# Optimization experiments

Hardware: AMD Instinct MI355X
Metric: run time of the kernel (lower is better)

## Reference

```python
import jax, jax.numpy as jnp
import numpy as np

# Broyden low-rank inverse-Jacobian matvecs. Us: [b,d,e,T], VTs: [b,T,d,e], x: [b,d,e].
# Unwritten history slots are zero, so using the full buffers equals torch's :nstep slicing.

def _matvec(Us, VTs, x):
    VTx = jnp.einsum('btde,bde->bt', VTs, x)
    return -x + jnp.einsum('bdet,bt->bde', Us, VTx)

def _rmatvec(Us, VTs, x):
    xTU = jnp.einsum('bde,bdet->bt', x, Us)
    return -x + jnp.einsum('bt,btde->bde', xTU, VTs)

def broyden(g, x0, threshold, eps):
    """Faithful port of broyden(..., ls=False): line search returns s=1 always."""
    B, D, E = x0.shape
    T = min(threshold, 27)
    gx0 = g(x0)
    init_obj = jnp.linalg.norm(gx0)
    protect = init_obj * (1e6 * E)  # protect_thres = 1e6 * n_elem
    Us0 = jnp.zeros((B, D, E, T), x0.dtype)
    VTs0 = jnp.zeros((B, T, D, E), x0.dtype)

    def cond(s):
        nstep, x, gx, upd, Us, VTs, obj, low, lx, lg = s
        return (obj >= eps) & (nstep < threshold) & (obj <= protect)

    def body(s):
        nstep, x, gx, upd, Us, VTs, obj, low, lx, lg = s
        x_new = x + upd                     # step size s = 1 (ls off)
        gx_new = g(x_new)
        dx, dg = upd, gx_new - gx
        nstep = nstep + 1
        obj_new = jnp.linalg.norm(gx_new)
        better = obj_new < low
        low = jnp.where(better, obj_new, low)
        lx = jnp.where(better, x_new, lx)
        lg = jnp.where(better, gx_new, lg)
        # Broyden rank-1 update of the inverse-Jacobian history
        vT = _rmatvec(Us, VTs, dx)
        denom = jnp.einsum('bde,bde->b', vT, dg)
        u = (dx - _matvec(Us, VTs, dg)) / denom[:, None, None]
        vT = jnp.where(jnp.isnan(vT), 0.0, vT)
        u = jnp.where(jnp.isnan(u), 0.0, u)
        Us = Us.at[:, :, :, (nstep - 1) % T].set(u)
        VTs = VTs.at[:, (nstep - 1) % T].set(vT)
        upd = -_matvec(Us, VTs, gx_new)
        return (nstep, x_new, gx_new, upd, Us, VTs, obj_new, low, lx, lg)

    s0 = (jnp.int32(0), x0, gx0, gx0, Us0, VTs0, init_obj, init_obj, x0, gx0)
    s = jax.lax.while_loop(cond, body, s0)
    return s[8], jnp.linalg.norm(s[9])  # lowest_xest, ||lowest_gx||


def f_layer(z, x, W, U, b):
    return jnp.tanh(z @ W + x @ U + b)


def setup_inputs() -> dict:
    key = jax.random.key(0)
    k1, k2, k3, k4 = jax.random.split(key, 4)
    B, D = 256, 2048
    x = jax.random.normal(k1, (B, D), jnp.float32)
    initial_point = jnp.zeros((B, D), jnp.float32)
    W = jax.random.normal(k2, (D, D), jnp.float32) * (0.4 / np.sqrt(D))  # contractive in z
    U = jax.random.normal(k3, (D, D), jnp.float32) * (1.0 / np.sqrt(D))
    b = jax.random.normal(k4, (D,), jnp.float32) * 0.01
    return {"x": x, "initial_point": initial_point, "W": W, "U": U, "b": b}


def reference(x, initial_point, W, U, b):
    MAX_ITER = 12  # kwargs['max_iter']
    B = x.shape[0]

    def g(z_flat):  # broyd_output_test: f(z, x) - z, flattened to [B, D, 1]
        z = z_flat[..., 0]
        return (f_layer(z, x, W, U, b) - z)[..., None]

    z0 = initial_point.reshape(B, -1, 1)
    out_x, _ = broyden(g, z0, MAX_ITER, 1e-8)
    z = f_layer(out_x[..., 0].reshape(x.shape), x, W, U, b)
    return z
```

## Files before the change

kernel.cpp:

```cpp
#include <hip/hip_runtime.h>
#include <math.h>


#define DD 2048
#define KA 4096
#define KW 2048
#define BB 256
#define BD (BB * DD)
#define TT 12
#define NKS 4

#define ST_S   0
#define ST_A   169
#define ST_B   325
#define ST_PHI 481
#define ST_XI  494
#define ST_XSN 507
#define ST_SZ  1024

typedef unsigned short ushort_t;
typedef _Float16 half_t;
typedef __attribute__((ext_vector_type(8))) short short8;
typedef __attribute__((ext_vector_type(4))) float floatx4;
typedef __attribute__((ext_vector_type(4))) _Float16 half4;

__device__ __forceinline__ ushort_t f2bf(float f) {
    unsigned int u = __float_as_uint(f);
    unsigned int r = (u + 0x7FFFu + ((u >> 16) & 1u)) >> 16;
    return (ushort_t)r;
}
__device__ __forceinline__ float bf2f(ushort_t h) {
    return __uint_as_float(((unsigned int)h) << 16);
}
__device__ __forceinline__ void gload_lds16(const void* g, void* l) {
    __builtin_amdgcn_global_load_lds(
        (const __attribute__((address_space(1))) unsigned int*)g,
        (__attribute__((address_space(3))) unsigned int*)l, 16, 0, 0);
}
__device__ __forceinline__ float wave_red(float v) {
#pragma unroll
    for (int off = 32; off > 0; off >>= 1) v += __shfl_down(v, off, 64);
    return v;
}

__global__ __launch_bounds__(256)
void prep(const float* __restrict__ W, const float* __restrict__ U,
          ushort_t* __restrict__ Wt, ushort_t* __restrict__ Ut,
          const float* __restrict__ xin, ushort_t* __restrict__ Axx,
          float* __restrict__ stbase) {
    __shared__ ushort_t Hs[64][65];
    const int bid = blockIdx.x;
    const int tid = threadIdx.x;
    if (bid < 2048) {
        const int bz = bid >> 10, by = (bid >> 5) & 31, bx = bid & 31;
        const float* src = bz ? U : W;
        ushort_t* dst = bz ? Ut : Wt;
        const int k0 = by * 64, n0 = bx * 64;
        const int r = tid >> 4, c4 = (tid & 15) * 4;
#pragma unroll
        for (int i = 0; i < 4; ++i) {
            int kr = r + i * 16;
            float4 w = *(const float4*)(src + (size_t)(k0 + kr) * DD + n0 + c4);
            Hs[kr][c4 + 0] = f2bf(w.x); Hs[kr][c4 + 1] = f2bf(w.y);
            Hs[kr][c4 + 2] = f2bf(w.z); Hs[kr][c4 + 3] = f2bf(w.w);
        }
        __syncthreads();
#pragma unroll
        for (int i = 0; i < 4; ++i) {
            int nr = r + i * 16;
            ushort4 hv = { Hs[c4+0][nr], Hs[c4+1][nr], Hs[c4+2][nr], Hs[c4+3][nr] };
            *(ushort4*)(dst + (size_t)(n0 + nr) * KW + (size_t)(k0 + c4)) = hv;
        }
    } else {
        const int i4 = (bid - 2048) * 256 + tid;
        const int idx = i4 * 4;
        const int m = idx >> 11, col = idx & 2047;
        float4 xv = ((const float4*)xin)[i4];
        float a[4] = {xv.x, xv.y, xv.z, xv.w};
        ushort_t hh[4], ll[4];
#pragma unroll
        for (int j = 0; j < 4; ++j) { hh[j] = f2bf(a[j]); ll[j] = f2bf(a[j] - bf2f(hh[j])); }
        ushort4 h = {hh[0],hh[1],hh[2],hh[3]}, l = {ll[0],ll[1],ll[2],ll[3]};
        size_t ab = (size_t)m * KA + col;
        *(ushort4*)(Axx + ab) = h; *(ushort4*)(Axx + ab + DD) = l;
        if (i4 < 65544) {
            float4 z = {0.f, 0.f, 0.f, 0.f};
            ((float4*)stbase)[i4] = z;
        }
    }
}

template<int LDA, int KSLICE, int NIT, int BMOD, typename YT>
__global__ __launch_bounds__(512)
void gemm_t(const ushort_t* __restrict__ A, const ushort_t* __restrict__ Bt,
            YT* __restrict__ y) {
    __shared__ ushort_t As[2][128 * 64];
    __shared__ ushort_t Bs[2][64 * 64];
    const int tid = threadIdx.x;
    const int lane = tid & 63, w = tid >> 6;
    const int bn = blockIdx.x * 64;
    const int mt = blockIdx.y;
    const int ks = blockIdx.z;
    const int waveM = w >> 1, waveN = w & 1;

    const int srow = tid >> 3;
    const int sg = (tid & 7) ^ (srow & 7);
    const ushort_t* Ag = A  + (size_t)(mt * 128 + srow) * LDA + ks * KSLICE + sg * 8;
    const ushort_t* Bg = Bt + (size_t)(bn + srow) * KW + (ks & BMOD) * KSLICE + sg * 8;
    const size_t rs64 = (size_t)64 * LDA;

    const int q = lane >> 4, rl = lane & 15;
    int offA[2][2], offB[2][2];
#pragma unroll
    for (int kk = 0; kk < 2; ++kk) {
        int j = kk * 4 + q;
#pragma unroll
        for (int mi = 0; mi < 2; ++mi) {
            int m = waveM * 32 + mi * 16 + rl;
            offA[kk][mi] = (m * 8 + (j ^ (m & 7))) * 8;
        }
#pragma unroll
        for (int ni = 0; ni < 2; ++ni) {
            int n = waveN * 32 + ni * 16 + rl;
            offB[kk][ni] = (n * 8 + (j ^ (n & 7))) * 8;
        }
    }

    floatx4 acc[2][2];
#pragma unroll
    for (int mi = 0; mi < 2; ++mi)
#pragma unroll
        for (int ni = 0; ni < 2; ++ni) acc[mi][ni] = (floatx4){0.f,0.f,0.f,0.f};

    gload_lds16(Ag,        As[0] + tid * 8);
    gload_lds16(Ag + rs64, As[0] + (512 + tid) * 8);
    gload_lds16(Bg,        Bs[0] + tid * 8);
    Ag += 64; Bg += 64;
    __syncthreads();

    for (int it = 0; it < NIT; ++it) {
        const int cur = it & 1, nxt = cur ^ 1;
        if (it + 1 < NIT) {
            gload_lds16(Ag,        As[nxt] + tid * 8);
            gload_lds16(Ag + rs64, As[nxt] + (512 + tid) * 8);
            gload_lds16(Bg,        Bs[nxt] + tid * 8);
            Ag += 64; Bg += 64;
        }
        const ushort_t* Ab = As[cur];
        const ushort_t* Bb = Bs[cur];
#pragma unroll
        for (int kk = 0; kk < 2; ++kk) {
            short8 b0 = *(const short8*)(Bb + offB[kk][0]);
            short8 b1 = *(const short8*)(Bb + offB[kk][1]);
#pragma unroll
            for (int mi = 0; mi < 2; ++mi) {
                short8 a = *(const short8*)(Ab + offA[kk][mi]);
                acc[mi][0] = __builtin_amdgcn_mfma_f32_16x16x32_bf16(a, b0, acc[mi][0], 0, 0, 0);
                acc[mi][1] = __builtin_amdgcn_mfma_f32_16x16x32_bf16(a, b1, acc[mi][1], 0, 0, 0);
            }
        }
        __syncthreads();
    }

    YT* yp = y + (size_t)ks * BD;
    const int mb = mt * 128 + waveM * 32 + q * 4;
    const int nb = bn + waveN * 32 + rl;
#pragma unroll
    for (int mi = 0; mi < 2; ++mi)
#pragma unroll
        for (int r = 0; r < 4; ++r) {
            yp[(size_t)(mb + mi * 16 + r) * DD + nb]      = (YT)acc[mi][0][r];
            yp[(size_t)(mb + mi * 16 + r) * DD + nb + 16] = (YT)acc[mi][1][r];
        }
}

__global__ __launch_bounds__(512)
void epi0(const float* __restrict__ y, const float* __restrict__ bias,
          float* __restrict__ c, ushort_t* __restrict__ gxp,
          ushort_t* __restrict__ Azz, float* __restrict__ state,
          float* __restrict__ scal) {
    __shared__ float red[8];
    const int tid = threadIdx.x;
    const int b = blockIdx.x;
    const int col = tid * 4;
    const size_t base = (size_t)b * DD + col;

    float4 cc = *(const float4*)(bias + col);
#pragma unroll
    for (int s = 0; s < NKS; ++s) {
        float4 v = *(const float4*)(y + (size_t)s * BD + base);
        cc.x += v.x; cc.y += v.y; cc.z += v.z; cc.w += v.w;
    }
    *(float4*)(c + base) = cc;
    float4 g = { tanhf(cc.x), tanhf(cc.y), tanhf(cc.z), tanhf(cc.w) };
    ushort4 gs = { f2bf(g.x), f2bf(g.y), f2bf(g.z), f2bf(g.w) };
    *(ushort4*)(gxp + base) = gs;
    *(ushort4*)(Azz + base) = gs;

    float pd = g.x*g.x + g.y*g.y + g.z*g.z + g.w*g.w;
    pd = wave_red(pd);
    if ((tid & 63) == 0) red[tid >> 6] = pd;
    __syncthreads();
    if (tid == 0) {
        float t = 0.f;
#pragma unroll
        for (int w2 = 0; w2 < 8; ++w2) t += red[w2];
        float* stb = state + (size_t)b * ST_SZ;
        stb[ST_S + 0]   = t;
        stb[ST_PHI + 0] = 1.f;
        stb[ST_XI + 0]  = 1.f;
        atomicAdd(&scal[0], t);
    }
}

__global__ __launch_bounds__(512)
void broyden_gram(const half_t* __restrict__ yh, const float* __restrict__ c,
                  ushort_t* __restrict__ gxp, ushort_t* __restrict__ Azz,
                  float* __restrict__ state, float* __restrict__ scal, int k)
{
    __shared__ float red[8][16];
    __shared__ float dots[14];
    __shared__ float Sl[169], Al[156], Bl[156], PHl[13], XIl[13];
    __shared__ float newA[14], newB[14], nphi[14];
    __shared__ double dyv[13], dxtu[12], dvdg[12], dcgx[13], dden[1];
    const int tid = threadIdx.x;
    const int lane = tid & 63, w = tid >> 6;
    const int b = blockIdx.x;
    const int p = k - 1;
    float* stb = state + (size_t)b * ST_SZ;

    for (int i = tid; i < 169; i += 512) Sl[i] = stb[ST_S + i];
    for (int i = tid; i < 156; i += 512) { Al[i] = stb[ST_A + i]; Bl[i] = stb[ST_B + i]; }
    if (tid < 13) { PHl[tid] = stb[ST_PHI + tid]; XIl[tid] = stb[ST_XI + tid]; }

    const int col = tid * 4;
    const size_t base = (size_t)b * DD + col;
    float4 pre = *(const float4*)(c + base);
#pragma unroll
    for (int s = 0; s < NKS; ++s) {
        half4 v = *(const half4*)(yh + (size_t)s * BD + base);
        pre.x += (float)v.x; pre.y += (float)v.y;
        pre.z += (float)v.z; pre.w += (float)v.w;
    }

    float4 G[12];
#pragma unroll
    for (int j = 0; j < 12; ++j)
        if (j < k) {
            ushort4 gu = *(const ushort4*)(gxp + (size_t)j * BD + base);
            G[j] = (float4){ bf2f(gu.x), bf2f(gu.y), bf2f(gu.z), bf2f(gu.w) };
        }

    __syncthreads();

    float4 x = {0.f, 0.f, 0.f, 0.f};
#pragma unroll
    for (int j = 0; j < 12; ++j)
        if (j < k) {
            float xc = XIl[j];
            x.x = fmaf(xc, G[j].x, x.x); x.y = fmaf(xc, G[j].y, x.y);
            x.z = fmaf(xc, G[j].z, x.z); x.w = fmaf(xc, G[j].w, x.w);
        }
    float4 gk = { tanhf(pre.x) - x.x, tanhf(pre.y) - x.y,
                  tanhf(pre.z) - x.z, tanhf(pre.w) - x.w };

#pragma unroll
    for (int j = 0; j < 12; ++j)
        if (j < k) {
            float pd = G[j].x*gk.x + G[j].y*gk.y + G[j].z*gk.z + G[j].w*gk.w;
            pd = wave_red(pd);
            if (lane == 0) red[w][j] = pd;
        }
    {
        float pdk = gk.x*gk.x + gk.y*gk.y + gk.z*gk.z + gk.w*gk.w;
        pdk = wave_red(pdk);
        if (lane == 0) red[w][k] = pdk;
    }
    __syncthreads();
    if (tid <= k) {
        float s = 0.f;
#pragma unroll
        for (int w2 = 0; w2 < 8; ++w2) s += red[w2][tid];
        dots[tid] = s;
        if (tid == k) atomicAdd(&scal[k], s);
    }
    __syncthreads();

    if (tid < k) {
        double s = 0.0;
        for (int j = 0; j < k; ++j) s += (double)Sl[tid*13 + j] * (double)PHl[j];
        dyv[tid] = s;
    }
    __syncthreads();
    if (tid < p) {
        double sx = 0.0, sv = 0.0;
        for (int j = 0; j < k; ++j) {
            sx += (double)Al[tid*13 + j] * dyv[j];
            sv += (double)Bl[tid*13 + j] * ((double)dots[j] - (double)Sl[j*13 + (k-1)]);
        }
        dxtu[tid] = sx; dvdg[tid] = sv;
    }
    __syncthreads();
    if (tid < k) {
        double s = -(double)PHl[tid];
        for (int t = 0; t < p; ++t) s += dxtu[t] * (double)Bl[t*13 + tid];
        newB[tid] = (float)s;
    }
    __syncthreads();
    if (tid == 0) {
        double s = 0.0;
        for (int j = 0; j < k; ++j)
            s += (double)newB[j] * ((double)dots[j] - (double)Sl[j*13 + (k-1)]);
        dden[0] = s;
    }
    __syncthreads();
    if (tid <= k) {
        double s = (double)((tid < 13) ? PHl[tid] : 0.f);
        if (tid == k)     s += 1.0;
        if (tid == k - 1) s -= 1.0;
        for (int t = 0; t < p; ++t) s -= dvdg[t] * (double)Al[t*13 + tid];
        newA[tid] = (float)(s / dden[0]);
    }
    if (tid >= 32 && tid < 32 + p) {
        int t = tid - 32;
        double s = 0.0;
        for (int j = 0; j < k; ++j) s += (double)Bl[t*13 + j] * (double)dots[j];
        dcgx[t] = s;
    }
    if (tid == 63) {
        double s = 0.0;
        for (int j = 0; j < k; ++j) s += (double)newB[j] * (double)dots[j];
        dcgx[p] = s;
    }
    __syncthreads();
    if (tid <= k) {
        double s = (tid == k) ? 1.0 : 0.0;
        for (int t = 0; t < p; ++t) s -= dcgx[t] * (double)Al[t*13 + tid];
        s -= dcgx[p] * (double)newA[tid];
        nphi[tid] = (float)s;
    }
    __syncthreads();

    if (tid <= k) {
        stb[ST_S + k*13 + tid] = dots[tid];
        stb[ST_S + tid*13 + k] = dots[tid];
        stb[ST_A + p*13 + tid] = newA[tid];
        stb[ST_PHI + tid] = nphi[tid];
        float xi_old = (tid < 13) ? XIl[tid] : 0.f;
        stb[ST_XI + tid] = xi_old + nphi[tid];
    }
    if (tid < k) stb[ST_B + p*13 + tid] = newB[tid];
    if (tid < 13) stb[ST_XSN + k*13 + tid] = XIl[tid];

    {
        ushort4 gs = { f2bf(gk.x), f2bf(gk.y), f2bf(gk.z), f2bf(gk.w) };
        *(ushort4*)(gxp + (size_t)k * BD + base) = gs;
    }

    if (k < TT) {
        float4 xn = x;
#pragma unroll
        for (int j = 0; j < 12; ++j)
            if (j < k) {
                float fc = nphi[j];
                xn.x = fmaf(fc, G[j].x, xn.x); xn.y = fmaf(fc, G[j].y, xn.y);
                xn.z = fmaf(fc, G[j].z, xn.z); xn.w = fmaf(fc, G[j].w, xn.w);
            }
        float fk = nphi[k];
        xn.x = fmaf(fk, gk.x, xn.x); xn.y = fmaf(fk, gk.y, xn.y);
        xn.z = fmaf(fk, gk.z, xn.z); xn.w = fmaf(fk, gk.w, xn.w);

        ushort4 h = { f2bf(xn.x), f2bf(xn.y), f2bf(xn.z), f2bf(xn.w) };
        *(ushort4*)(Azz + base) = h;
    }
}

__global__ __launch_bounds__(256)
void final_out(const ushort_t* __restrict__ gxp, const float* __restrict__ state,
               const float* __restrict__ scal, float* __restrict__ out) {
    const int i4 = blockIdx.x * 256 + threadIdx.x;
    float best = scal[0];
    int bk = 0;
#pragma unroll
    for (int k = 1; k <= TT; ++k) {
        float o = scal[k];
        if (o < best) { best = o; bk = k; }
    }
    const size_t idx = (size_t)i4 * 4;
    const int m = (int)(idx >> 11);
    const float* cf = state + (size_t)m * ST_SZ + ST_XSN + bk * 13;
    ushort4 gb = *(const ushort4*)(gxp + (size_t)bk * BD + idx);
    float4 r = { bf2f(gb.x), bf2f(gb.y), bf2f(gb.z), bf2f(gb.w) };
    for (int j = 0; j < bk; ++j) {
        float c1 = cf[j];
        ushort4 gu = *(const ushort4*)(gxp + (size_t)j * BD + idx);
        r.x = fmaf(c1, bf2f(gu.x), r.x); r.y = fmaf(c1, bf2f(gu.y), r.y);
        r.z = fmaf(c1, bf2f(gu.z), r.z); r.w = fmaf(c1, bf2f(gu.w), r.w);
    }
    ((float4*)out)[i4] = r;
}

extern "C" void kernel_launch(void* const* d_in, const int* in_sizes, int n_in,
                              void* d_out, int out_size, void* d_ws, size_t ws_size,
                              hipStream_t stream) {
    const float* xin  = (const float*)d_in[0];
    const float* W    = (const float*)d_in[2];
    const float* U    = (const float*)d_in[3];
    const float* bias = (const float*)d_in[4];
    float* out = (float*)d_out;

    float* ws = (float*)d_ws;
    float* c      = ws;
    float* y      = ws + 1 * (size_t)BD;
    ushort_t* gxp = (ushort_t*)(ws + 9 * (size_t)BD);
    ushort_t* Axx = (ushort_t*)(ws + 16 * (size_t)BD);
    ushort_t* Azz = (ushort_t*)(ws + 17 * (size_t)BD);
    ushort_t* Wt  = (ushort_t*)(ws + 18 * (size_t)BD);
    ushort_t* Ut  = (ushort_t*)(ws + 22 * (size_t)BD);
    float* state  = ws + 26 * (size_t)BD;
    float* scal   = state + (size_t)BB * ST_SZ;

    prep<<<2560, 256, 0, stream>>>(W, U, Wt, Ut, xin, Axx, state);

    dim3 gg(32, 2, NKS);
    gemm_t<4096, 1024, 16, 1, float><<<gg, 512, 0, stream>>>(Axx, Ut, y);
    epi0<<<BB, 512, 0, stream>>>(y, bias, c, gxp, Azz, state, scal);

    for (int k = 1; k <= TT; ++k) {
        gemm_t<2048, 512, 8, 3, half_t><<<gg, 512, 0, stream>>>(Azz, Wt, (half_t*)y);
        broyden_gram<<<BB, 512, 0, stream>>>((const half_t*)y, c, gxp, Azz, state, scal, k);
    }

    final_out<<<512, 256, 0, stream>>>(gxp, state, scal, out);
}
```

Baseline: 349.0 us.

## Triple-buffer GEMM with smaller tiles and single-wave Broyden small solve

The GEMM tile drops from 128x64 to 64x64 with 256 threads, which doubles the grid. It switches to a three-stage LDS ring with explicit vmcnt waits and a single barrier per iteration, so loads run two stages ahead of compute. In broyden_gram, the small dense recurrence now runs in one wave using wave-local waits instead of many block-wide __syncthreads. The gxp loads and store are also reordered to overlap with the other loads. Smaller tiles reduce reuse but raise parallelism, and the wave-local sync relies on lgkmcnt plus wave_barrier being enough for LDS visibility.

```diff
diff --git a/kernel.cpp b/kernel.cpp
--- a/kernel.cpp
+++ b/kernel.cpp
@@ -42,6 +42,8 @@
     for (int off = 32; off > 0; off >>= 1) v += __shfl_down(v, off, 64);
     return v;
 }
+#define WS() do { asm volatile("s_waitcnt lgkmcnt(0)" ::: "memory"); \
+                  __builtin_amdgcn_wave_barrier(); } while (0)
 
 __global__ __launch_bounds__(256)
 void prep(const float* __restrict__ W, const float* __restrict__ U,
@@ -91,11 +93,11 @@
 }
 
 template<int LDA, int KSLICE, int NIT, int BMOD, typename YT>
-__global__ __launch_bounds__(512)
+__global__ __launch_bounds__(256)
 void gemm_t(const ushort_t* __restrict__ A, const ushort_t* __restrict__ Bt,
             YT* __restrict__ y) {
-    __shared__ ushort_t As[2][128 * 64];
-    __shared__ ushort_t Bs[2][64 * 64];
+    __shared__ ushort_t As[3][64 * 64];
+    __shared__ ushort_t Bs[3][64 * 64];
     const int tid = threadIdx.x;
     const int lane = tid & 63, w = tid >> 6;
     const int bn = blockIdx.x * 64;
@@ -105,9 +107,10 @@
 
     const int srow = tid >> 3;
     const int sg = (tid & 7) ^ (srow & 7);
-    const ushort_t* Ag = A  + (size_t)(mt * 128 + srow) * LDA + ks * KSLICE + sg * 8;
+    const ushort_t* Ag = A  + (size_t)(mt * 64 + srow) * LDA + ks * KSLICE + sg * 8;
     const ushort_t* Bg = Bt + (size_t)(bn + srow) * KW + (ks & BMOD) * KSLICE + sg * 8;
-    const size_t rs64 = (size_t)64 * LDA;
+    const size_t rsA = (size_t)32 * LDA;
+    const size_t rsB = (size_t)32 * KW;
 
     const int q = lane >> 4, rl = lane & 15;
     int offA[2][2], offB[2][2];
@@ -132,22 +135,32 @@
 #pragma unroll
         for (int ni = 0; ni < 2; ++ni) acc[mi][ni] = (floatx4){0.f,0.f,0.f,0.f};
 
-    gload_lds16(Ag,        As[0] + tid * 8);
-    gload_lds16(Ag + rs64, As[0] + (512 + tid) * 8);
-    gload_lds16(Bg,        Bs[0] + tid * 8);
+    gload_lds16(Ag,       As[0] + tid * 8);
+    gload_lds16(Ag + rsA, As[0] + (256 + tid) * 8);
+    gload_lds16(Bg,       Bs[0] + tid * 8);
+    gload_lds16(Bg + rsB, Bs[0] + (256 + tid) * 8);
     Ag += 64; Bg += 64;
-    __syncthreads();
-
+    gload_lds16(Ag,       As[1] + tid * 8);
+    gload_lds16(Ag + rsA, As[1] + (256 + tid) * 8);
+    gload_lds16(Bg,       Bs[1] + tid * 8);
+    gload_lds16(Bg + rsB, Bs[1] + (256 + tid) * 8);
+    Ag += 64; Bg += 64;
+
+#pragma unroll
     for (int it = 0; it < NIT; ++it) {
-        const int cur = it & 1, nxt = cur ^ 1;
-        if (it + 1 < NIT) {
-            gload_lds16(Ag,        As[nxt] + tid * 8);
-            gload_lds16(Ag + rs64, As[nxt] + (512 + tid) * 8);
-            gload_lds16(Bg,        Bs[nxt] + tid * 8);
+        if (it + 1 < NIT) asm volatile("s_waitcnt vmcnt(4)" ::: "memory");
+        else              asm volatile("s_waitcnt vmcnt(0)" ::: "memory");
+        __builtin_amdgcn_s_barrier();
+        if (it + 2 < NIT) {
+            const int nb3 = (it + 2) % 3;
+            gload_lds16(Ag,       As[nb3] + tid * 8);
+            gload_lds16(Ag + rsA, As[nb3] + (256 + tid) * 8);
+            gload_lds16(Bg,       Bs[nb3] + tid * 8);
+            gload_lds16(Bg + rsB, Bs[nb3] + (256 + tid) * 8);
             Ag += 64; Bg += 64;
         }
-        const ushort_t* Ab = As[cur];
-        const ushort_t* Bb = Bs[cur];
+        const ushort_t* Ab = As[it % 3];
+        const ushort_t* Bb = Bs[it % 3];
 #pragma unroll
         for (int kk = 0; kk < 2; ++kk) {
             short8 b0 = *(const short8*)(Bb + offB[kk][0]);
@@ -159,11 +172,10 @@
                 acc[mi][1] = __builtin_amdgcn_mfma_f32_16x16x32_bf16(a, b1, acc[mi][1], 0, 0, 0);
             }
         }
-        __syncthreads();
     }
 
     YT* yp = y + (size_t)ks * BD;
-    const int mb = mt * 128 + waveM * 32 + q * 4;
+    const int mb = mt * 64 + waveM * 32 + q * 4;
     const int nb = bn + waveN * 32 + rl;
 #pragma unroll
     for (int mi = 0; mi < 2; ++mi)
@@ -229,12 +241,17 @@
     const int p = k - 1;
     float* stb = state + (size_t)b * ST_SZ;
 
-    for (int i = tid; i < 169; i += 512) Sl[i] = stb[ST_S + i];
-    for (int i = tid; i < 156; i += 512) { Al[i] = stb[ST_A + i]; Bl[i] = stb[ST_B + i]; }
-    if (tid < 13) { PHl[tid] = stb[ST_PHI + tid]; XIl[tid] = stb[ST_XI + tid]; }
-
     const int col = tid * 4;
     const size_t base = (size_t)b * DD + col;
+
+    float4 G[12];
+#pragma unroll
+    for (int j = 0; j < 12; ++j)
+        if (j < k) {
+            ushort4 gu = *(const ushort4*)(gxp + (size_t)j * BD + base);
+            G[j] = (float4){ bf2f(gu.x), bf2f(gu.y), bf2f(gu.z), bf2f(gu.w) };
+        }
+
     float4 pre = *(const float4*)(c + base);
 #pragma unroll
     for (int s = 0; s < NKS; ++s) {
@@ -243,13 +260,9 @@
         pre.z += (float)v.z; pre.w += (float)v.w;
     }
 
-    float4 G[12];
-#pragma unroll
-    for (int j = 0; j < 12; ++j)
-        if (j < k) {
-            ushort4 gu = *(const ushort4*)(gxp + (size_t)j * BD + base);
-            G[j] = (float4){ bf2f(gu.x), bf2f(gu.y), bf2f(gu.z), bf2f(gu.w) };
-        }
+    for (int i = tid; i < 169; i += 512) Sl[i] = stb[ST_S + i];
+    for (int i = tid; i < 156; i += 512) { Al[i] = stb[ST_A + i]; Bl[i] = stb[ST_B + i]; }
+    if (tid < 13) { PHl[tid] = stb[ST_PHI + tid]; XIl[tid] = stb[ST_XI + tid]; }
 
     __syncthreads();
 
@@ -264,6 +277,11 @@
     float4 gk = { tanhf(pre.x) - x.x, tanhf(pre.y) - x.y,
                   tanhf(pre.z) - x.z, tanhf(pre.w) - x.w };
 
+    {
+        ushort4 gs = { f2bf(gk.x), f2bf(gk.y), f2bf(gk.z), f2bf(gk.w) };
+        *(ushort4*)(gxp + (size_t)k * BD + base) = gs;
+    }
+
 #pragma unroll
     for (int j = 0; j < 12; ++j)
         if (j < k) {
@@ -277,85 +295,82 @@
         if (lane == 0) red[w][k] = pdk;
     }
     __syncthreads();
-    if (tid <= k) {
-        float s = 0.f;
-#pragma unroll
-        for (int w2 = 0; w2 < 8; ++w2) s += red[w2][tid];
-        dots[tid] = s;
-        if (tid == k) atomicAdd(&scal[k], s);
+
+    if (w == 0) {
+        if (lane <= k) {
+            float s = 0.f;
+#pragma unroll
+            for (int w2 = 0; w2 < 8; ++w2) s += red[w2][lane];
+            dots[lane] = s;
+            if (lane == k) atomicAdd(&scal[k], s);
+        }
+        WS();
+        if (lane < k) {
+            double s = 0.0;
+            for (int j = 0; j < k; ++j) s += (double)Sl[lane*13 + j] * (double)PHl[j];
+            dyv[lane] = s;
+        }
+        WS();
+        if (lane < p) {
+            double sx = 0.0, sv = 0.0;
+            for (int j = 0; j < k; ++j) {
+                sx += (double)Al[lane*13 + j] * dyv[j];
+                sv += (double)Bl[lane*13 + j] * ((double)dots[j] - (double)Sl[j*13 + (k-1)]);
+            }
+            dxtu[lane] = sx; dvdg[lane] = sv;
+        }
+        WS();
+        if (lane < k) {
+            double s = -(double)PHl[lane];
+            for (int t = 0; t < p; ++t) s += dxtu[t] * (double)Bl[t*13 + lane];
+            newB[lane] = (float)s;
+        }
+        WS();
+        if (lane == 0) {
+            double s = 0.0;
+            for (int j = 0; j < k; ++j)
+                s += (double)newB[j] * ((double)dots[j] - (double)Sl[j*13 + (k-1)]);
+            dden[0] = s;
+        }
+        if (lane >= 32 && lane < 32 + p) {
+            int t = lane - 32;
+            double s = 0.0;
+            for (int j = 0; j < k; ++j) s += (double)Bl[t*13 + j] * (double)dots[j];
+            dcgx[t] = s;
+        }
+        if (lane == 63) {
+            double s = 0.0;
+            for (int j = 0; j < k; ++j) s += (double)newB[j] * (double)dots[j];
+            dcgx[p] = s;
+        }
+        WS();
+        if (lane <= k) {
+            double s = (double)((lane < 13) ? PHl[lane] : 0.f);
+            if (lane == k)     s += 1.0;
+            if (lane == k - 1) s -= 1.0;
+            for (int t = 0; t < p; ++t) s -= dvdg[t] * (double)Al[t*13 + lane];
+            newA[lane] = (float)(s / dden[0]);
+        }
+        WS();
+        if (lane <= k) {
+            double s = (lane == k) ? 1.0 : 0.0;
+            for (int t = 0; t < p; ++t) s -= dcgx[t] * (double)Al[t*13 + lane];
+            s -= dcgx[p] * (double)newA[lane];
+            nphi[lane] = (float)s;
+        }
+        WS();
+        if (lane <= k) {
+            stb[ST_S + k*13 + lane] = dots[lane];
+            stb[ST_S + lane*13 + k] = dots[lane];
+            stb[ST_A + p*13 + lane] = newA[lane];
+            stb[ST_PHI + lane] = nphi[lane];
+            float xi_old = (lane < 13) ? XIl[lane] : 0.f;
+            stb[ST_XI + lane] = xi_old + nphi[lane];
+        }
+        if (lane < k) stb[ST_B + p*13 + lane] = newB[lane];
+        if (lane < 13) stb[ST_XSN + k*13 + lane] = XIl[lane];
     }
     __syncthreads();
-
-    if (tid < k) {
-        double s = 0.0;
-        for (int j = 0; j < k; ++j) s += (double)Sl[tid*13 + j] * (double)PHl[j];
-        dyv[tid] = s;
-    }
-    __syncthreads();
-    if (tid < p) {
-        double sx = 0.0, sv = 0.0;
-        for (int j = 0; j < k; ++j) {
-            sx += (double)Al[tid*13 + j] * dyv[j];
-            sv += (double)Bl[tid*13 + j] * ((double)dots[j] - (double)Sl[j*13 + (k-1)]);
-        }
-        dxtu[tid] = sx; dvdg[tid] = sv;
-    }
-    __syncthreads();
-    if (tid < k) {
-        double s = -(double)PHl[tid];
-        for (int t = 0; t < p; ++t) s += dxtu[t] * (double)Bl[t*13 + tid];
-        newB[tid] = (float)s;
-    }
-    __syncthreads();
-    if (tid == 0) {
-        double s = 0.0;
-        for (int j = 0; j < k; ++j)
-            s += (double)newB[j] * ((double)dots[j] - (double)Sl[j*13 + (k-1)]);
-        dden[0] = s;
-    }
-    __syncthreads();
-    if (tid <= k) {
-        double s = (double)((tid < 13) ? PHl[tid] : 0.f);
-        if (tid == k)     s += 1.0;
-        if (tid == k - 1) s -= 1.0;
-        for (int t = 0; t < p; ++t) s -= dvdg[t] * (double)Al[t*13 + tid];
-        newA[tid] = (float)(s / dden[0]);
-    }
-    if (tid >= 32 && tid < 32 + p) {
-        int t = tid - 32;
-        double s = 0.0;
-        for (int j = 0; j < k; ++j) s += (double)Bl[t*13 + j] * (double)dots[j];
-        dcgx[t] = s;
-    }
-    if (tid == 63) {
-        double s = 0.0;
-        for (int j = 0; j < k; ++j) s += (double)newB[j] * (double)dots[j];
-        dcgx[p] = s;
-    }
-    __syncthreads();
-    if (tid <= k) {
-        double s = (tid == k) ? 1.0 : 0.0;
-        for (int t = 0; t < p; ++t) s -= dcgx[t] * (double)Al[t*13 + tid];
-        s -= dcgx[p] * (double)newA[tid];
-        nphi[tid] = (float)s;
-    }
-    __syncthreads();
-
-    if (tid <= k) {
-        stb[ST_S + k*13 + tid] = dots[tid];
-        stb[ST_S + tid*13 + k] = dots[tid];
-        stb[ST_A + p*13 + tid] = newA[tid];
-        stb[ST_PHI + tid] = nphi[tid];
-        float xi_old = (tid < 13) ? XIl[tid] : 0.f;
-        stb[ST_XI + tid] = xi_old + nphi[tid];
-    }
-    if (tid < k) stb[ST_B + p*13 + tid] = newB[tid];
-    if (tid < 13) stb[ST_XSN + k*13 + tid] = XIl[tid];
-
-    {
-        ushort4 gs = { f2bf(gk.x), f2bf(gk.y), f2bf(gk.z), f2bf(gk.w) };
-        *(ushort4*)(gxp + (size_t)k * BD + base) = gs;
-    }
 
     if (k < TT) {
         float4 xn = x;
@@ -422,12 +437,12 @@
 
     prep<<<2560, 256, 0, stream>>>(W, U, Wt, Ut, xin, Axx, state);
 
-    dim3 gg(32, 2, NKS);
-    gemm_t<4096, 1024, 16, 1, float><<<gg, 512, 0, stream>>>(Axx, Ut, y);
+    dim3 gg(32, 4, NKS);
+    gemm_t<4096, 1024, 16, 1, float><<<gg, 256, 0, stream>>>(Axx, Ut, y);
     epi0<<<BB, 512, 0, stream>>>(y, bias, c, gxp, Azz, state, scal);
 
     for (int k = 1; k <= TT; ++k) {
-        gemm_t<2048, 512, 8, 3, half_t><<<gg, 512, 0, stream>>>(Azz, Wt, (half_t*)y);
+        gemm_t<2048, 512, 8, 3, half_t><<<gg, 256, 0, stream>>>(Azz, Wt, (half_t*)y);
         broyden_gram<<<BB, 512, 0, stream>>>((const half_t*)y, c, gxp, Azz, state, scal, k);
     }
 
```

After: 327.9 us. 6.0% less time.
